# Optimization experiments

Hardware: AMD Instinct MI355X
Metric: run time of the kernel (lower is better)

Reference implementation:

```python
import jax, jax.numpy as jnp
import numpy as np

TEMP = 0.1
EPS = 1e-12  # torch F.normalize eps


def _normalize(v):
    return v / jnp.maximum(jnp.linalg.norm(v, axis=1, keepdims=True), EPS)


def _scale_loss(a1, a2, b1, c1):
    # diag of exp(a1 @ a2.T / temp): computed directly from paired rows
    # (same math as eye-mask + row-sum in the original).
    diag = jnp.exp(jnp.sum(a1 * a2, axis=1) / TEMP)            # [B]
    denom = (jnp.exp(a1 @ b1.T / TEMP).sum(1, keepdims=True)
             + jnp.exp(a1 @ c1.T / TEMP).sum(1, keepdims=True))  # [B,1]
    # NOTE: [B] / [B,1] broadcasts to [B,B], exactly as in the torch code.
    return jnp.mean(-jnp.log(diag / denom))


def setup_inputs() -> dict:
    key = jax.random.key(0)
    kx, ky, kz = jax.random.split(key, 3)
    shape = (8192, 128)
    return {
        "x": jax.random.normal(kx, shape, dtype=jnp.float32),
        "y": jax.random.normal(ky, shape, dtype=jnp.float32),
        "z": jax.random.normal(kz, shape, dtype=jnp.float32),
    }


def reference(x, y, z):
    x = _normalize(x)
    y = _normalize(y)
    z = _normalize(z)
    B = x.shape[0] // 2
    x1, x2 = x[:B], x[B:]
    y1, y2 = y[:B], y[B:]
    z1, z2 = z[:B], z[B:]

    loss_scale = (_scale_loss(x1, x2, y1, z1)
                  + _scale_loss(y1, y2, x1, z1)
                  + _scale_loss(z1, z2, x1, y1))

    xyz1 = jnp.concatenate([x1, y1, z1], axis=1)  # [B, 3D]
    xyz2 = jnp.concatenate([x2, y2, z2], axis=1)
    m = jnp.exp(xyz1 @ xyz2.T / TEMP)             # [B, B]
    # [B] / [B,1] -> [B,B] broadcast, matching the torch code.
    loss_view = jnp.mean(-jnp.log(jnp.diagonal(m) / m.sum(1, keepdims=True)))

    return loss_view + loss_scale
```

## Files before the change

### kernel.cpp

```cpp
#include <hip/hip_runtime.h>
#include <hip/hip_bf16.h>

#define BHALF 4096
#define DDIM 128
#define KCAT 384
#define TEMP_INV 10.0f

typedef __attribute__((ext_vector_type(8))) short short8;
typedef __attribute__((ext_vector_type(4))) float f32x4;

__device__ __forceinline__ void gload16(const ushort* g, ushort* l) {
  __builtin_amdgcn_global_load_lds(
      (const __attribute__((address_space(1))) unsigned int*)g,
      (__attribute__((address_space(3))) unsigned int*)l, 16, 0, 0);
}

__global__ __launch_bounds__(256) void norm_diag_kernel(
    const float* __restrict__ x, const float* __restrict__ y,
    const float* __restrict__ z, ushort* __restrict__ nrm1,
    ushort* __restrict__ nrm2, float* __restrict__ dxyz) {
  int wave = threadIdx.x >> 6;
  int lane = threadIdx.x & 63;
  int gi = blockIdx.x * 4 + wave;
  int mat = gi >> 12;
  int i = gi & 4095;
  const float* src = (mat == 0 ? x : (mat == 1 ? y : z));
  float2 a = *(const float2*)(src + (size_t)i * DDIM + lane * 2);
  float2 b = *(const float2*)(src + (size_t)(i + BHALF) * DDIM + lane * 2);
  float s1 = a.x * a.x + a.y * a.y;
  float s2 = b.x * b.x + b.y * b.y;
  float d = a.x * b.x + a.y * b.y;
#pragma unroll
  for (int m = 1; m < 64; m <<= 1) {
    s1 += __shfl_xor(s1, m, 64);
    s2 += __shfl_xor(s2, m, 64);
    d += __shfl_xor(d, m, 64);
  }
  float r1 = 1.0f / fmaxf(sqrtf(s1), 1e-12f);
  float r2 = 1.0f / fmaxf(sqrtf(s2), 1e-12f);
  ushort* d1 = nrm1 + (size_t)i * KCAT + mat * DDIM + lane * 2;
  ushort* d2 = nrm2 + (size_t)i * KCAT + mat * DDIM + lane * 2;
  __hip_bfloat162 o1, o2;
  o1.x = __float2bfloat16(a.x * r1);
  o1.y = __float2bfloat16(a.y * r1);
  o2.x = __float2bfloat16(b.x * r2);
  o2.y = __float2bfloat16(b.y * r2);
  *(__hip_bfloat162*)d1 = o1;
  *(__hip_bfloat162*)d2 = o2;
  if (lane == 0) dxyz[mat * BHALF + i] = d * r1 * r2;
}

__global__ __launch_bounds__(256) void gram_kernel(
    const ushort* __restrict__ nrm1, const ushort* __restrict__ nrm2,
    float* __restrict__ sums) {
  int g = blockIdx.z;
  const ushort* Abase;
  const ushort* Bbase;
  int K;
  float* rs;
  float* cs;
  if (g == 0) {
    Abase = nrm1; Bbase = nrm1 + 128; K = 128;
    rs = sums; cs = sums + 4096;
  } else if (g == 1) {
    Abase = nrm1; Bbase = nrm1 + 256; K = 128;
    rs = sums + 2 * 4096; cs = sums + 3 * 4096;
  } else if (g == 2) {
    Abase = nrm1 + 128; Bbase = nrm1 + 256; K = 128;
    rs = sums + 4 * 4096; cs = sums + 5 * 4096;
  } else {
    Abase = nrm1; Bbase = nrm2; K = 384;
    rs = sums + 6 * 4096; cs = nullptr;
  }

  __shared__ ushort As[128][32];
  __shared__ ushort Bs[128][32];

  int tid = threadIdx.x;
  int lane = tid & 63;
  int wave = tid >> 6;
  int wr = wave >> 1;
  int wc = wave & 1;

  int rowbase = blockIdx.x * 128;
  int colbase = blockIdx.y * 128;

  int lrow = lane >> 2;
  int lchunk8 = (((lane & 3) ^ ((lrow >> 1) & 3)) << 3);
  const ushort* gA0 =
      Abase + (size_t)(rowbase + wave * 16 + lrow) * KCAT + lchunk8;
  const ushort* gA1 = gA0 + (size_t)64 * KCAT;
  const ushort* gB0 =
      Bbase + (size_t)(colbase + wave * 16 + lrow) * KCAT + lchunk8;
  const ushort* gB1 = gB0 + (size_t)64 * KCAT;
  ushort* lA0 = &As[wave * 16][0];
  ushort* lA1 = &As[wave * 16 + 64][0];
  ushort* lB0 = &Bs[wave * 16][0];
  ushort* lB1 = &Bs[wave * 16 + 64][0];

  int rsel = lane & 15;
  int slot8 = (((lane >> 4) ^ ((rsel >> 1) & 3)) << 3);

  f32x4 acc[4][4] = {};

  int ksteps = K >> 5;
  for (int ks = 0; ks < ksteps; ++ks) {
    gload16(gA0, lA0);
    gload16(gA1, lA1);
    gload16(gB0, lB0);
    gload16(gB1, lB1);
    gA0 += 32; gA1 += 32; gB0 += 32; gB1 += 32;
    __syncthreads();
    short8 af[4], bf[4];
#pragma unroll
    for (int m = 0; m < 4; ++m)
      af[m] = *(const short8*)&As[wr * 64 + m * 16 + rsel][slot8];
#pragma unroll
    for (int n = 0; n < 4; ++n)
      bf[n] = *(const short8*)&Bs[wc * 64 + n * 16 + rsel][slot8];
#pragma unroll
    for (int m = 0; m < 4; ++m)
#pragma unroll
      for (int n = 0; n < 4; ++n)
        acc[m][n] = __builtin_amdgcn_mfma_f32_16x16x32_bf16(af[m], bf[n],
                                                            acc[m][n], 0, 0, 0);
    __syncthreads();
  }

#pragma unroll
  for (int m = 0; m < 4; ++m)
#pragma unroll
    for (int n = 0; n < 4; ++n)
#pragma unroll
      for (int r = 0; r < 4; ++r)
        acc[m][n][r] = __expf(acc[m][n][r] * TEMP_INV);

#pragma unroll
  for (int m = 0; m < 4; ++m) {
    float rsum[4];
#pragma unroll
    for (int r = 0; r < 4; ++r)
      rsum[r] = acc[m][0][r] + acc[m][1][r] + acc[m][2][r] + acc[m][3][r];
#pragma unroll
    for (int r = 0; r < 4; ++r) {
      rsum[r] += __shfl_xor(rsum[r], 1, 64);
      rsum[r] += __shfl_xor(rsum[r], 2, 64);
      rsum[r] += __shfl_xor(rsum[r], 4, 64);
      rsum[r] += __shfl_xor(rsum[r], 8, 64);
    }
    if ((lane & 15) == 0) {
      int rbase = rowbase + wr * 64 + m * 16 + (lane >> 4) * 4;
#pragma unroll
      for (int r = 0; r < 4; ++r) atomicAdd(&rs[rbase + r], rsum[r]);
    }
  }

  if (cs != nullptr) {
#pragma unroll
    for (int n = 0; n < 4; ++n) {
      float csum = 0.0f;
#pragma unroll
      for (int m = 0; m < 4; ++m)
#pragma unroll
        for (int r = 0; r < 4; ++r) csum += acc[m][n][r];
      csum += __shfl_xor(csum, 16, 64);
      csum += __shfl_xor(csum, 32, 64);
      if (lane < 16) atomicAdd(&cs[colbase + wc * 64 + n * 16 + lane], csum);
    }
  }
}

__global__ __launch_bounds__(1024) void loss_kernel(
    const float* __restrict__ sums, const float* __restrict__ dxyz,
    float* __restrict__ out) {
  const float* rs0 = sums;
  const float* cs0 = sums + 4096;
  const float* rs1 = sums + 2 * 4096;
  const float* cs1 = sums + 3 * 4096;
  const float* rs2 = sums + 4 * 4096;
  const float* cs2 = sums + 5 * 4096;
  const float* rs3 = sums + 6 * 4096;
  int tid = threadIdx.x;
  float acc = 0.0f;
  for (int i = tid; i < BHALF; i += 1024) {
    float dxv = dxyz[i];
    float dyv = dxyz[4096 + i];
    float dzv = dxyz[2 * 4096 + i];
    float lx = logf(rs0[i] + rs1[i]) - TEMP_INV * dxv;
    float ly = logf(cs0[i] + rs2[i]) - TEMP_INV * dyv;
    float lz = logf(cs1[i] + cs2[i]) - TEMP_INV * dzv;
    float lv = logf(rs3[i]) - TEMP_INV * (dxv + dyv + dzv);
    acc += lx + ly + lz + lv;
  }
  __shared__ float red[16];
#pragma unroll
  for (int m = 1; m < 64; m <<= 1) acc += __shfl_xor(acc, m, 64);
  if ((tid & 63) == 0) red[tid >> 6] = acc;
  __syncthreads();
  if (tid == 0) {
    float t = 0.0f;
#pragma unroll
    for (int i = 0; i < 16; ++i) t += red[i];
    out[0] = t * (1.0f / 4096.0f);
  }
}

extern "C" void kernel_launch(void* const* d_in, const int* in_sizes, int n_in,
                              void* d_out, int out_size, void* d_ws,
                              size_t ws_size, hipStream_t stream) {
  const float* x = (const float*)d_in[0];
  const float* y = (const float*)d_in[1];
  const float* z = (const float*)d_in[2];
  char* ws = (char*)d_ws;
  ushort* nrm1 = (ushort*)ws;
  ushort* nrm2 = nrm1 + (size_t)BHALF * KCAT;
  float* sums = (float*)(ws + 2 * (size_t)BHALF * KCAT * sizeof(ushort));
  float* dxyz = sums + 7 * 4096;

  hipMemsetAsync(sums, 0, 7 * 4096 * sizeof(float), stream);
  norm_diag_kernel<<<3 * BHALF / 4, 256, 0, stream>>>(x, y, z, nrm1, nrm2,
                                                      dxyz);
  gram_kernel<<<dim3(32, 32, 4), 256, 0, stream>>>(nrm1, nrm2, sums);
  loss_kernel<<<1, 1024, 0, stream>>>(sums, dxyz, (float*)d_out);
}
```

Before: 77.47 us.

## Double-buffer LDS tiles in gram kernel to overlap global loads with MFMA

The gram kernel now keeps two LDS stages for the A and B tiles and issues the global-to-LDS loads for the next K step before computing on the current one. It waits with a manual vmcnt so only the current stage must be complete, and uses raw s_barrier plus sched_barrier instead of __syncthreads. This is meant to hide global load latency behind the MFMA work, which matters little when the K loop has only 4 to 12 steps. The manual waitcnt and barrier placement risks ordering bugs, since LDS reads are not explicitly waited on before the buffer is overwritten.

```diff
diff --git a/kernel.cpp b/kernel.cpp
--- a/kernel.cpp
+++ b/kernel.cpp
@@ -73,8 +73,8 @@
     rs = sums + 6 * 4096; cs = nullptr;
   }
 
-  __shared__ ushort As[128][32];
-  __shared__ ushort Bs[128][32];
+  __shared__ ushort As[2][128][32];
+  __shared__ ushort Bs[2][128][32];
 
   int tid = threadIdx.x;
   int lane = tid & 63;
@@ -87,16 +87,10 @@
 
   int lrow = lane >> 2;
   int lchunk8 = (((lane & 3) ^ ((lrow >> 1) & 3)) << 3);
-  const ushort* gA0 =
+  const ushort* gA =
       Abase + (size_t)(rowbase + wave * 16 + lrow) * KCAT + lchunk8;
-  const ushort* gA1 = gA0 + (size_t)64 * KCAT;
-  const ushort* gB0 =
+  const ushort* gB =
       Bbase + (size_t)(colbase + wave * 16 + lrow) * KCAT + lchunk8;
-  const ushort* gB1 = gB0 + (size_t)64 * KCAT;
-  ushort* lA0 = &As[wave * 16][0];
-  ushort* lA1 = &As[wave * 16 + 64][0];
-  ushort* lB0 = &Bs[wave * 16][0];
-  ushort* lB1 = &Bs[wave * 16 + 64][0];
 
   int rsel = lane & 15;
   int slot8 = (((lane >> 4) ^ ((rsel >> 1) & 3)) << 3);
@@ -104,28 +98,45 @@
   f32x4 acc[4][4] = {};
 
   int ksteps = K >> 5;
-  for (int ks = 0; ks < ksteps; ++ks) {
-    gload16(gA0, lA0);
-    gload16(gA1, lA1);
-    gload16(gB0, lB0);
-    gload16(gB1, lB1);
-    gA0 += 32; gA1 += 32; gB0 += 32; gB1 += 32;
-    __syncthreads();
+
+#define STAGE(b, t)                                        \
+  do {                                                     \
+    const ushort* a_ = gA + (t) * 32;                      \
+    const ushort* b_ = gB + (t) * 32;                      \
+    gload16(a_, &As[(b)][wave * 16][0]);                   \
+    gload16(a_ + (size_t)64 * KCAT, &As[(b)][wave * 16 + 64][0]); \
+    gload16(b_, &Bs[(b)][wave * 16][0]);                   \
+    gload16(b_ + (size_t)64 * KCAT, &Bs[(b)][wave * 16 + 64][0]); \
+  } while (0)
+
+  STAGE(0, 0);
+  for (int t = 0; t < ksteps; ++t) {
+    int cur = t & 1;
+    if (t + 1 < ksteps) {
+      STAGE(cur ^ 1, t + 1);
+      asm volatile("s_waitcnt vmcnt(4)" ::: "memory");
+    } else {
+      asm volatile("s_waitcnt vmcnt(0)" ::: "memory");
+    }
+    __builtin_amdgcn_s_barrier();
+    __builtin_amdgcn_sched_barrier(0);
     short8 af[4], bf[4];
 #pragma unroll
     for (int m = 0; m < 4; ++m)
-      af[m] = *(const short8*)&As[wr * 64 + m * 16 + rsel][slot8];
+      af[m] = *(const short8*)&As[cur][wr * 64 + m * 16 + rsel][slot8];
 #pragma unroll
     for (int n = 0; n < 4; ++n)
-      bf[n] = *(const short8*)&Bs[wc * 64 + n * 16 + rsel][slot8];
+      bf[n] = *(const short8*)&Bs[cur][wc * 64 + n * 16 + rsel][slot8];
 #pragma unroll
     for (int m = 0; m < 4; ++m)
 #pragma unroll
       for (int n = 0; n < 4; ++n)
         acc[m][n] = __builtin_amdgcn_mfma_f32_16x16x32_bf16(af[m], bf[n],
                                                             acc[m][n], 0, 0, 0);
-    __syncthreads();
-  }
+    __builtin_amdgcn_sched_barrier(0);
+    __builtin_amdgcn_s_barrier();
+  }
+#undef STAGE
 
 #pragma unroll
   for (int m = 0; m < 4; ++m)
```

New measurement: 81.71 us. +5.5%, slower.
